# Kernel tuning notes

Measured on AMD Instinct MI355X. Metric: run time of the kernel, lower is better.

## Reference

```python
import jax, jax.numpy as jnp
import numpy as np
from jax import lax

B, N, C = 8, 16384, 4
NUM_GROUPS = 128
GROUP_SIZE = 32
GROUP_RADIUS = 0.1
UPSCALE_K = 128
OVERLAP_FACTOR = 0.7


def setup_inputs() -> dict:
    key = jax.random.key(0)
    k1, k2 = jax.random.split(key)
    # xyz in [0,1]^3, energy in [0,1] at channel 3
    points = jax.random.uniform(k1, (B, N, C), dtype=jnp.float32)
    lengths = jax.random.randint(k2, (B,), N // 2, N + 1).astype(jnp.int32)
    return {"points": points, "lengths": lengths}


def _fps(xyz, lengths, K):
    """Farthest point sampling. xyz: (B,N,3) -> centers (B,K,3), idx (B,K)."""
    B_, N_, _ = xyz.shape
    valid = jnp.arange(N_)[None, :] < lengths[:, None]          # (B,N)
    mind0 = jnp.where(valid, jnp.inf, -jnp.inf)                 # running min dist
    start = jnp.zeros((B_,), jnp.int32)                         # fixed start point
    batch = jnp.arange(B_)

    def step(carry, _):
        mind, cur = carry
        c = xyz[batch, cur]                                     # (B,3)
        d = jnp.sum((xyz - c[:, None, :]) ** 2, axis=-1)        # (B,N)
        mind = jnp.minimum(mind, jnp.where(valid, d, -jnp.inf))
        nxt = jnp.argmax(mind, axis=1).astype(jnp.int32)
        return (mind, nxt), cur

    _, idxs = lax.scan(step, (mind0, start), None, length=K)
    idxs = idxs.T                                               # (B,K)
    centers = xyz[batch[:, None], idxs]                         # (B,K,3)
    return centers, idxs


def _cnms(centers, radius, overlap_factor):
    """Greedy cluster-NMS over FPS-ordered centers. Returns keep mask (B,G)."""
    B_, G, _ = centers.shape
    d2 = jnp.sum((centers[:, :, None, :] - centers[:, None, :, :]) ** 2, axis=-1)
    thr = (2.0 * radius * (1.0 - overlap_factor)) ** 2          # spheres overlap > factor

    def step(keep, j):
        conflict = jnp.any(keep & (d2[:, j, :] < thr), axis=-1)
        keep = keep.at[:, j].set(~conflict)
        return keep, None

    keep, _ = lax.scan(step, jnp.zeros((B_, G), bool), jnp.arange(G))
    return keep


def _ball_query(centers, xyz, lengths, retain, K, radius):
    """First-K points within radius of each center (pytorch3d semantics); -1 pad."""
    N_ = xyz.shape[1]
    d2 = jnp.sum((centers[:, :, None, :] - xyz[:, None, :, :]) ** 2, axis=-1)  # (B,G,N)
    in_len = (jnp.arange(N_)[None, :] < lengths[:, None])[:, None, :]
    valid = (d2 <= radius * radius) & in_len & retain[:, :, None]
    # pick the K smallest point indices among valid ones -> "first K found"
    key_ = jnp.where(valid, jnp.arange(N_, dtype=jnp.int32)[None, None, :], N_)
    negv, _ = lax.top_k(-key_, K)                               # (B,G,K)
    idx = -negv
    return jnp.where(idx == N_, -1, idx)


def reference(points, lengths):
    xyz = points[..., :3]
    centers, _ = _fps(xyz, lengths, NUM_GROUPS)                 # (B,G,3)
    retain = _cnms(centers, GROUP_RADIUS, OVERLAP_FACTOR)       # (B,G)
    idx = _ball_query(centers, xyz, lengths, retain, UPSCALE_K, GROUP_RADIUS)

    # select_topk_by_energy (energies_idx = 3)
    batch = jnp.arange(points.shape[0])[:, None, None]
    invalid = idx == -1
    energies = jnp.where(invalid, -jnp.inf, points[batch, jnp.clip(idx, 0), 3])
    topv, topi = lax.top_k(energies, GROUP_SIZE)                # (B,G,K_new)
    tidx = jnp.take_along_axis(idx, topi, axis=2)
    tidx = jnp.where(jnp.isneginf(topv), -1, tidx)

    # fill_empty_indices: replace -1 with the group's first index
    fidx = jnp.where(tidx == -1, tidx[:, :, :1], tidx)

    # masked_gather: -1 -> gather 0 then zero out
    groups = points[batch, jnp.clip(fidx, 0)]                   # (B,G,K,C)
    groups = jnp.where((fidx == -1)[..., None], 0.0, groups)

    group_lengths = jnp.sum(jnp.all(tidx != -1, axis=2), axis=1)  # (B,)
    embedding_mask = jnp.arange(NUM_GROUPS)[None, :] < group_lengths[:, None]

    # center xyz channels, then scale ALL channels by radius (as in source)
    groups = groups.at[..., :3].add(-centers[:, :, None, :])
    groups = groups / GROUP_RADIUS
    return groups, centers, embedding_mask
```

## Files before the change

### kernel.cpp

```cpp
#include <hip/hip_runtime.h>
#include <math.h>

#define B_ 8
#define N_ 16384
#define G_ 128
#define GS_ 32
#define UK_ 128
#define FPS_T 1024
#define FPS_W 16
#define PPT 16
#define BQ_T 512
#define BQ_W 8

typedef float v2f __attribute__((ext_vector_type(2)));

#define PK_ADD(d, a, b) asm("v_pk_add_f32 %0, %1, %2" : "=v"(d) : "v"(a), "v"(b))
#define PK_MUL(d, a, b) asm("v_pk_mul_f32 %0, %1, %2" : "=v"(d) : "v"(a), "v"(b))

#define DPP64_MAXSTEP(vv, ctrl, rmask)                                          \
  {                                                                             \
    unsigned _lo = (unsigned)__builtin_amdgcn_update_dpp(                       \
        0, (int)(unsigned)((vv) & 0xffffffffull), (ctrl), (rmask), 0xf, false); \
    unsigned _hi = (unsigned)__builtin_amdgcn_update_dpp(                       \
        0, (int)(unsigned)((vv) >> 32), (ctrl), (rmask), 0xf, false);           \
    unsigned long long _tv = ((unsigned long long)_hi << 32) | _lo;             \
    if (_tv > (vv)) (vv) = _tv;                                                 \
  }

__device__ __forceinline__ float dist2(float x, float y, float z,
                                       float cx, float cy, float cz) {
    float dx = __fsub_rn(x, cx);
    float dy = __fsub_rn(y, cy);
    float dz = __fsub_rn(z, cz);
    return __fadd_rn(__fadd_rn(__fmul_rn(dx, dx), __fmul_rn(dy, dy)),
                     __fmul_rn(dz, dz));
}

__global__ void init_kernel(int* __restrict__ gl) {
    int t = threadIdx.x;
    if (t < B_) gl[t] = 0;
}

__global__ __launch_bounds__(FPS_T, 4) void fps_cnms_kernel(
    const float4* __restrict__ pts, const int* __restrict__ lengths,
    float* __restrict__ centers_out, int* __restrict__ keep_out) {
    const int b = blockIdx.x;
    const int t = threadIdx.x;
    const int lane = t & 63;
    const int wv = t >> 6;
    const int len = lengths[b];
    const float4* p = pts + (size_t)b * N_;

    __shared__ __align__(16) unsigned long long s_part[2][FPS_W];
    __shared__ float s_cen[G_][3];

    v2f xp[PPT / 2], yp[PPT / 2], zp[PPT / 2];
    float mind[PPT];
#pragma unroll
    for (int j = 0; j < PPT / 2; j++) {
        int nA = (2 * j) * FPS_T + t;
        int nB = nA + FPS_T;
        float4 qA = p[nA];
        float4 qB = p[nB];
        v2f xx, yy, zz;
        xx.x = qA.x; xx.y = qB.x;
        yy.x = qA.y; yy.y = qB.y;
        zz.x = qA.z; zz.y = qB.z;
        xp[j] = xx; yp[j] = yy; zp[j] = zz;
        mind[2 * j]     = (nA < len) ? INFINITY : -INFINITY;
        mind[2 * j + 1] = (nB < len) ? INFINITY : -INFINITY;
    }
#pragma unroll
    for (int j = 0; j < PPT / 2; j++) {
        asm volatile("" : "+v"(xp[j]), "+v"(yp[j]), "+v"(zp[j]));
    }

    int n = 0;
    for (int k = 0; k < G_; k++) {
        float4 c = p[n];
        if (t == 0) {
            centers_out[(b * G_ + k) * 3 + 0] = c.x;
            centers_out[(b * G_ + k) * 3 + 1] = c.y;
            centers_out[(b * G_ + k) * 3 + 2] = c.z;
            s_cen[k][0] = c.x; s_cen[k][1] = c.y; s_cen[k][2] = c.z;
        }
        if (k == G_ - 1) break;

        float ncx = -c.x, ncy = -c.y, ncz = -c.z;
        v2f cX, cY, cZ;
        cX.x = ncx; cX.y = ncx;
        cY.x = ncy; cY.y = ncy;
        cZ.x = ncz; cZ.y = ncz;

        float bv = -INFINITY;
        int bi = 0;
#pragma unroll
        for (int j = 0; j < PPT / 2; j++) {
            v2f dx, dy, dz, qx, qy, qz, s0, d2v;
            PK_ADD(dx, xp[j], cX);
            PK_ADD(dy, yp[j], cY);
            PK_ADD(dz, zp[j], cZ);
            PK_MUL(qx, dx, dx);
            PK_MUL(qy, dy, dy);
            PK_MUL(qz, dz, dz);
            PK_ADD(s0, qx, qy);
            PK_ADD(d2v, s0, qz);
            float mA = fminf(mind[2 * j],     d2v.x);
            float mB = fminf(mind[2 * j + 1], d2v.y);
            mind[2 * j] = mA;
            mind[2 * j + 1] = mB;
            if (mA > bv) { bv = mA; bi = 2 * j; }
            if (mB > bv) { bv = mB; bi = 2 * j + 1; }
        }

        unsigned u = __float_as_uint(bv);
        u = (u & 0x80000000u) ? ~u : (u | 0x80000000u);
        int bn = (bi << 10) | t;
        unsigned long long v = ((unsigned long long)u << 32) | (unsigned)(~bn);

        DPP64_MAXSTEP(v, 0x111, 0xf);
        DPP64_MAXSTEP(v, 0x112, 0xf);
        DPP64_MAXSTEP(v, 0x114, 0xf);
        DPP64_MAXSTEP(v, 0x118, 0xf);
        DPP64_MAXSTEP(v, 0x142, 0xa);
        DPP64_MAXSTEP(v, 0x143, 0xc);
        if (lane == 63) s_part[k & 1][wv] = v;
        __syncthreads();

        unsigned long long m = s_part[k & 1][lane & 15];
        DPP64_MAXSTEP(m, 0x111, 0xf);
        DPP64_MAXSTEP(m, 0x112, 0xf);
        DPP64_MAXSTEP(m, 0x114, 0xf);
        DPP64_MAXSTEP(m, 0x118, 0xf);
        unsigned wlo = (unsigned)__builtin_amdgcn_readlane(
            (int)(unsigned)(m & 0xffffffffull), 15);
        n = (int)(~wlo);
    }

    __syncthreads();

    if (t < 64) {
        const float THR = (float)((2.0 * 0.1 * (1.0 - 0.7)) * (2.0 * 0.1 * (1.0 - 0.7)));
        float ax = s_cen[t][0],      ay = s_cen[t][1],      az = s_cen[t][2];
        float ex = s_cen[t + 64][0], ey = s_cen[t + 64][1], ez = s_cen[t + 64][2];
        bool k0 = false, k1 = false;
        for (int j = 0; j < G_; j++) {
            float jx = s_cen[j][0], jy = s_cen[j][1], jz = s_cen[j][2];
            bool c0 = k0 && (dist2(ax, ay, az, jx, jy, jz) < THR);
            bool c1 = k1 && (dist2(ex, ey, ez, jx, jy, jz) < THR);
            bool conflict = __any(c0 || c1);
            if (j == t)      k0 = !conflict;
            if (j == t + 64) k1 = !conflict;
        }
        keep_out[b * G_ + t]      = k0 ? 1 : 0;
        keep_out[b * G_ + t + 64] = k1 ? 1 : 0;
    }
}

__global__ __launch_bounds__(BQ_T) void group_kernel(
    const float4* __restrict__ pts, const int* __restrict__ lengths,
    const float* __restrict__ centers, const int* __restrict__ keep,
    float* __restrict__ groups_out, int* __restrict__ gl) {
    const int bid = blockIdx.x;
    const int b = bid >> 7;
    const int t = threadIdx.x;
    const int lane = t & 63;
    const int wv = t >> 6;

    const float cx = centers[bid * 3 + 0];
    const float cy = centers[bid * 3 + 1];
    const float cz = centers[bid * 3 + 2];
    float4* out4 = (float4*)(groups_out + (size_t)bid * GS_ * 4);

    if (!keep[bid]) {
        if (t < GS_) {
            float4 o;
            o.x = __fdiv_rn(__fsub_rn(0.f, cx), 0.1f);
            o.y = __fdiv_rn(__fsub_rn(0.f, cy), 0.1f);
            o.z = __fdiv_rn(__fsub_rn(0.f, cz), 0.1f);
            o.w = 0.f;
            out4[t] = o;
        }
        return;
    }

    __shared__ int   s_widx[BQ_W][UK_];
    __shared__ float s_wen[BQ_W][UK_];
    __shared__ int   s_wcnt[BQ_W];
    __shared__ int   s_list[UK_];
    __shared__ float s_en[UK_];
    __shared__ int   s_ord[GS_];

    const int len = lengths[b];
    const float R2 = (float)(0.1 * 0.1);
    const float4* p = pts + (size_t)b * N_;

    {
        const int base0 = wv * (N_ / BQ_W);
        int cnt = 0;
        for (int it = 0; it < (N_ / BQ_W) / 64; it++) {
            int n = base0 + it * 64 + lane;
            float4 q = p[n];
            float d2 = dist2(q.x, q.y, q.z, cx, cy, cz);
            bool pred = (n < len) && (d2 <= R2);
            unsigned long long m = __ballot(pred);
            int prefix = __popcll(m & ((1ull << lane) - 1ull));
            int slot = cnt + prefix;
            if (pred && slot < UK_) { s_widx[wv][slot] = n; s_wen[wv][slot] = q.w; }
            cnt += __popcll(m);
        }
        if (lane == 0) s_wcnt[wv] = (cnt < UK_) ? cnt : UK_;
    }
    __syncthreads();

    int M = 0;
#pragma unroll
    for (int w = 0; w < BQ_W; w++) M += s_wcnt[w];
    if (M > UK_) M = UK_;

    if (t < UK_ && t < M) {
        int j = t, w = 0;
        while (w < BQ_W - 1 && j >= s_wcnt[w]) { j -= s_wcnt[w]; w++; }
        s_list[t] = s_widx[w][j];
        s_en[t]   = s_wen[w][j];
    }
    __syncthreads();

    if (wv == 0) {
        float v0 = (lane < M) ? s_en[lane] : -INFINITY;
        float v1 = (lane + 64 < M) ? s_en[lane + 64] : -INFINITY;
        for (int k = 0; k < GS_; k++) {
            float bv; int bs;
            if (v0 >= v1) { bv = v0; bs = lane; }
            else          { bv = v1; bs = lane + 64; }
#pragma unroll
            for (int off = 32; off; off >>= 1) {
                float ov = __shfl_xor(bv, off);
                int   os = __shfl_xor(bs, off);
                bool tk = (ov > bv) || (ov == bv && os < bs);
                bv = tk ? ov : bv; bs = tk ? os : bs;
            }
            if (lane == 0) s_ord[k] = (bv == -INFINITY) ? -1 : bs;
            if (bs == lane)           v0 = -INFINITY;
            else if (bs == lane + 64) v1 = -INFINITY;
        }
    }
    __syncthreads();

    if (t < GS_) {
        int o0 = s_ord[0];
        int first = (o0 >= 0) ? s_list[o0] : -1;
        int ok = s_ord[t];
        int ti = (ok >= 0) ? s_list[ok] : -1;
        int f = (ti == -1) ? first : ti;
        float px = 0.f, py = 0.f, pz = 0.f, pw = 0.f;
        if (f >= 0) { float4 q = p[f]; px = q.x; py = q.y; pz = q.z; pw = q.w; }
        float4 o;
        o.x = __fdiv_rn(__fsub_rn(px, cx), 0.1f);
        o.y = __fdiv_rn(__fsub_rn(py, cy), 0.1f);
        o.z = __fdiv_rn(__fsub_rn(pz, cz), 0.1f);
        o.w = __fdiv_rn(pw, 0.1f);
        out4[t] = o;
    }
    if (t == 0 && M >= GS_) atomicAdd(&gl[b], 1);
}

__global__ void mask_kernel(const int* __restrict__ gl, float* __restrict__ mask_out) {
    int t = threadIdx.x;
    int b = t >> 7, g = t & 127;
    mask_out[t] = (g < gl[b]) ? 1.0f : 0.0f;
}

extern "C" void kernel_launch(void* const* d_in, const int* in_sizes, int n_in,
                              void* d_out, int out_size, void* d_ws, size_t ws_size,
                              hipStream_t stream) {
    const float4* pts = (const float4*)d_in[0];
    const int* lengths = (const int*)d_in[1];
    float* out = (float*)d_out;
    float* groups = out;
    float* centers = out + (size_t)B_ * G_ * GS_ * 4;
    float* mask = centers + (size_t)B_ * G_ * 3;
    int* keep = (int*)d_ws;
    int* gl = keep + B_ * G_;

    hipLaunchKernelGGL(init_kernel, dim3(1), dim3(64), 0, stream, gl);
    hipLaunchKernelGGL(fps_cnms_kernel, dim3(B_), dim3(FPS_T), 0, stream,
                       pts, lengths, centers, keep);
    hipLaunchKernelGGL(group_kernel, dim3(B_ * G_), dim3(BQ_T), 0, stream,
                       pts, lengths, centers, keep, groups, gl);
    hipLaunchKernelGGL(mask_kernel, dim3(1), dim3(B_ * G_), 0, stream, gl, mask);
}
```

Measured before the change: 347.2 us.

## Move FPS x/y coordinates to LDS and split argmax into max then index

```diff
diff --git a/kernel.cpp b/kernel.cpp
--- a/kernel.cpp
+++ b/kernel.cpp
@@ -51,29 +51,29 @@
     const int len = lengths[b];
     const float4* p = pts + (size_t)b * N_;
 
+    __shared__ float4 s_xy4[N_ / 2];
     __shared__ __align__(16) unsigned long long s_part[2][FPS_W];
     __shared__ float s_cen[G_][3];
 
-    v2f xp[PPT / 2], yp[PPT / 2], zp[PPT / 2];
-    float mind[PPT];
+    v2f zp[PPT / 2];
+    v2f mp[PPT / 2];
 #pragma unroll
     for (int j = 0; j < PPT / 2; j++) {
         int nA = (2 * j) * FPS_T + t;
         int nB = nA + FPS_T;
         float4 qA = p[nA];
         float4 qB = p[nB];
-        v2f xx, yy, zz;
-        xx.x = qA.x; xx.y = qB.x;
-        yy.x = qA.y; yy.y = qB.y;
-        zz.x = qA.z; zz.y = qB.z;
-        xp[j] = xx; yp[j] = yy; zp[j] = zz;
-        mind[2 * j]     = (nA < len) ? INFINITY : -INFINITY;
-        mind[2 * j + 1] = (nB < len) ? INFINITY : -INFINITY;
-    }
-#pragma unroll
-    for (int j = 0; j < PPT / 2; j++) {
-        asm volatile("" : "+v"(xp[j]), "+v"(yp[j]), "+v"(zp[j]));
-    }
+        s_xy4[j * FPS_T + t] = make_float4(qA.x, qB.x, qA.y, qB.y);
+        v2f zz; zz.x = qA.z; zz.y = qB.z;
+        zp[j] = zz;
+        v2f mm;
+        mm.x = (nA < len) ? INFINITY : -INFINITY;
+        mm.y = (nB < len) ? INFINITY : -INFINITY;
+        mp[j] = mm;
+    }
+#pragma unroll
+    for (int j = 0; j < PPT / 2; j++) asm volatile("" : "+v"(zp[j]));
+    __syncthreads();
 
     int n = 0;
     for (int k = 0; k < G_; k++) {
@@ -86,31 +86,41 @@
         }
         if (k == G_ - 1) break;
 
-        float ncx = -c.x, ncy = -c.y, ncz = -c.z;
-        v2f cX, cY, cZ;
-        cX.x = ncx; cX.y = ncx;
-        cY.x = ncy; cY.y = ncy;
-        cZ.x = ncz; cZ.y = ncz;
-
-        float bv = -INFINITY;
-        int bi = 0;
+        v2f cXX, cYY, cZZ;
+        cXX.x = -c.x; cXX.y = -c.x;
+        cYY.x = -c.y; cYY.y = -c.y;
+        cZZ.x = -c.z; cZZ.y = -c.z;
+
 #pragma unroll
         for (int j = 0; j < PPT / 2; j++) {
+            float4 xy = s_xy4[j * FPS_T + t];
+            v2f xv, yv;
+            xv.x = xy.x; xv.y = xy.y;
+            yv.x = xy.z; yv.y = xy.w;
             v2f dx, dy, dz, qx, qy, qz, s0, d2v;
-            PK_ADD(dx, xp[j], cX);
-            PK_ADD(dy, yp[j], cY);
-            PK_ADD(dz, zp[j], cZ);
+            PK_ADD(dx, xv, cXX);
+            PK_ADD(dy, yv, cYY);
+            PK_ADD(dz, zp[j], cZZ);
             PK_MUL(qx, dx, dx);
             PK_MUL(qy, dy, dy);
             PK_MUL(qz, dz, dz);
             PK_ADD(s0, qx, qy);
             PK_ADD(d2v, s0, qz);
-            float mA = fminf(mind[2 * j],     d2v.x);
-            float mB = fminf(mind[2 * j + 1], d2v.y);
-            mind[2 * j] = mA;
-            mind[2 * j + 1] = mB;
-            if (mA > bv) { bv = mA; bi = 2 * j; }
-            if (mB > bv) { bv = mB; bi = 2 * j + 1; }
+            mp[j].x = fminf(mp[j].x, d2v.x);
+            mp[j].y = fminf(mp[j].y, d2v.y);
+        }
+
+        float bv = mp[0].x;
+#pragma unroll
+        for (int j = 0; j < PPT / 2; j++) {
+            if (j > 0) bv = fmaxf(bv, mp[j].x);
+            bv = fmaxf(bv, mp[j].y);
+        }
+        int bi = 0;
+#pragma unroll
+        for (int s = PPT - 1; s >= 0; s--) {
+            float mv = (s & 1) ? mp[s >> 1].y : mp[s >> 1].x;
+            if (mv == bv) bi = s;
         }
 
         unsigned u = __float_as_uint(bv);
```

Result: faster. 337.2 us (-2.9%).
